# Performance work log

Measured on AMD Instinct MI355X. Metric: run time of the kernel, lower is better.

## Reference

```python
import jax, jax.numpy as jnp
import numpy as np

B, T, N, H = 32, 12, 1024, 64


def _norm_laplacian(A):
    # I - D^{-1/2} A D^{-1/2}
    d = A.sum(axis=1)
    d_is = jnp.where(d > 0, d ** -0.5, 0.0)
    return jnp.eye(A.shape[0], dtype=A.dtype) - d_is[:, None] * A * d_is[None, :]


def setup_inputs() -> dict:
    key = jax.random.key(0)
    ks = jax.random.split(key, 8)
    inputs = jax.random.normal(ks[0], (B, T, N), jnp.float32)
    states = jax.random.normal(ks[1], (T, B, N * H), jnp.float32) * 0.1
    dtw = jax.random.uniform(ks[2], (N, N), jnp.float32)
    adj = jax.random.uniform(ks[3], (N, N), jnp.float32)
    spectrum = jax.random.uniform(ks[4], (N, N), jnp.float32)
    time_delay = jax.random.normal(ks[5], (N, N), jnp.float32) * 10.0
    lim1 = (6.0 / (H + 1 + 2 * H)) ** 0.5  # xavier_uniform
    W1 = jax.random.uniform(ks[6], (H + 1, 2 * H), jnp.float32, -lim1, lim1)
    b1 = jnp.ones((2 * H,), jnp.float32)  # bias init 1.0 for conv1
    lim2 = (6.0 / (H + 1 + H)) ** 0.5
    W2 = jax.random.uniform(ks[7], (H + 1, H), jnp.float32, -lim2, lim2)
    b2 = jnp.zeros((H,), jnp.float32)
    return {"inputs": inputs, "states": states, "dtw": dtw, "adj": adj,
            "spectrum": spectrum, "time_delay": time_delay,
            "W1": W1, "b1": b1, "W2": W2, "b2": b2, "sample_rate": 5}


def reference(inputs, states, dtw, adj, spectrum, time_delay, W1, b1, W2, b2, sample_rate):
    Bs, Ts, Nn = inputs.shape
    Hh = W2.shape[1]
    I = jnp.eye(Nn, dtype=jnp.float32)
    L_adj = _norm_laplacian(adj)
    L_spec = _norm_laplacian(spectrum)
    # time_indicator = times - ceil(|td| / sample_rate)
    time_ind = jnp.float32(Ts) - jnp.ceil(jnp.abs(time_delay) / sample_rate)

    def gconv(A, x, h3, W, b):
        # x: [B,N], h3: [B,N,H'] -> [B, N*out]
        cat = jnp.concatenate([x[..., None], h3], axis=-1)          # [B,N,H'+1]
        a = jnp.einsum('mn,bnk->bmk', A, cat)                       # [B,N,H'+1]
        return (a @ W + b).reshape(Bs, -1)

    def step(carry, xs):
        gcn1, gcn2, _ = carry
        t, x, h = xs                                                # x:[B,N], h:[B,N*H]
        multi = t == Ts - 1
        dtwt = jnp.where((dtw != 0) & ((t + 1) > time_ind), dtw, 0.0)
        A = jnp.where(multi,
                      (dtwt + I + L_adj + L_spec) / 3.0,
                      (dtwt + L_spec + I) / 2.0)
        gcn1 = gcn1 + gconv(A, x, h.reshape(Bs, Nn, Hh), W1, b1)
        ru = jax.nn.sigmoid(gcn1)
        r, u = jnp.split(ru, 2, axis=1)
        gcn2 = gcn2 + gconv(A, x, (r * h).reshape(Bs, Nn, Hh), W2, b2)
        c = jnp.tanh(gcn2)
        h_new = u * h + (1.0 - u) * c
        return (gcn1, gcn2, h_new), None

    init = (jnp.zeros((Bs, Nn * 2 * Hh), jnp.float32),
            jnp.zeros((Bs, Nn * Hh), jnp.float32),
            jnp.zeros((Bs, Nn * Hh), jnp.float32))
    x_t = jnp.transpose(inputs, (1, 0, 2))                          # [T,B,N]
    (_, _, h_new), _ = jax.lax.scan(step, init, (jnp.arange(Ts), x_t, states))
    return (h_new, h_new)
```

## Files before the change

kernel.cpp:

```cpp
#include <hip/hip_runtime.h>
#include <math.h>

#define NN 1024
#define BB 32
#define TT 12
#define HH 64
#define K1 65
#define NCOLS (BB * K1)
#define BPAD 72
#define NC2 (BB * BPAD)
#define NH (NN * HH)
#define KX 1024
#define BM 128
#define BN 256
#define BKK 32
#define NBUF 3
#define PTS 264

typedef __attribute__((ext_vector_type(8))) _Float16 h8;
typedef __attribute__((ext_vector_type(4))) float f32x4;

__device__ __forceinline__ void gload16(const void* g, void* l) {
    __builtin_amdgcn_global_load_lds((__attribute__((address_space(1))) void*)g,
                                     (__attribute__((address_space(3))) void*)l,
                                     16, 0, 0);
}

__global__ void rowsum_rsqrt(const float* __restrict__ M, float* __restrict__ ds) {
    int row = blockIdx.x;
    const float* p = M + (size_t)row * NN;
    float s = 0.f;
    for (int i = threadIdx.x; i < NN; i += blockDim.x) s += p[i];
    __shared__ float red[256];
    red[threadIdx.x] = s;
    __syncthreads();
    for (int off = 128; off; off >>= 1) {
        if (threadIdx.x < off) red[threadIdx.x] += red[threadIdx.x + off];
        __syncthreads();
    }
    if (threadIdx.x == 0) {
        float d = red[0];
        ds[row] = d > 0.f ? 1.0f / sqrtf(d) : 0.f;
    }
}

__global__ void build_A2(const float* __restrict__ dtw, const float* __restrict__ adj,
                         const float* __restrict__ spec, const float* __restrict__ td,
                         const float* __restrict__ dsA, const float* __restrict__ dsS,
                         const int* __restrict__ sr_ptr, _Float16* __restrict__ A2) {
    int idx = blockIdx.x * blockDim.x + threadIdx.x;
    int m = idx >> 10, n = idx & 1023;
    float sr = (float)sr_ptr[0];
    float dtw_v = dtw[idx], adj_v = adj[idx], spec_v = spec[idx], td_v = td[idx];
    float I = (m == n) ? 1.f : 0.f;
    float Lspec = I - dsS[m] * spec_v * dsS[n];
    float Ladj  = I - dsA[m] * adj_v * dsA[n];
    float tind = (float)TT - ceilf(fabsf(td_v) / sr);
    float base2 = 0.5f * (Lspec + I);
    float base3 = (Lspec + Ladj + I) * (1.f / 3.f);
    bool nz = (dtw_v != 0.f);
#pragma unroll
    for (int t = 0; t < TT; ++t) {
        bool act = nz && ((float)(t + 1) > tind);
        float a = (t == TT - 1) ? base3 + (act ? dtw_v * (1.f / 3.f) : 0.f)
                                : base2 + (act ? dtw_v * 0.5f : 0.f);
        A2[((size_t)t * NN + m) * KX + n] = (_Float16)a;
    }
}

__global__ __launch_bounds__(256) void build_cat(
    const float* __restrict__ inputs, const float* __restrict__ states,
    const _Float16* __restrict__ rall, _Float16* __restrict__ cat,
    int tbase, int pass2) {
    __shared__ float hs[64][68];
    __shared__ float rs[64][68];
    const int z = blockIdx.z, t = tbase + z;
    const int b = blockIdx.y, nb = blockIdx.x;
    const int tid = threadIdx.x;
    const float* sb = states + ((size_t)t * BB + b) * NH + (size_t)nb * 4096;
    const float4* src = (const float4*)sb;
#pragma unroll
    for (int q = 0; q < 4; ++q) {
        float4 v = src[tid * 4 + q];
        int fi = tid * 16 + q * 4;
        *(float4*)&hs[fi >> 6][fi & 63] = v;
    }
    if (pass2) {
        const _Float16* rb = rall + ((size_t)t * BB + b) * NH + (size_t)nb * 4096;
#pragma unroll
        for (int i = 0; i < 16; ++i) {
            int fi = tid * 16 + i;
            rs[fi >> 6][fi & 63] = (float)rb[fi];
        }
    }
    __syncthreads();
    _Float16* catz = cat + (size_t)z * NC2 * KX;
    int jp = tid >> 2, ni = (tid & 3) << 4;
    int col = b * BPAD + 1 + jp;
    __attribute__((aligned(16))) _Float16 hib[16];
#pragma unroll
    for (int i = 0; i < 16; ++i) {
        float v = hs[ni + i][jp];
        if (pass2) v *= rs[ni + i][jp];
        hib[i] = (_Float16)v;
    }
    size_t dst = (size_t)col * KX + nb * 64 + ni;
    *(uint4*)(catz + dst)     = *(uint4*)&hib[0];
    *(uint4*)(catz + dst + 8) = *(uint4*)&hib[8];
    if (tid < 64) {
        float v = inputs[((size_t)b * TT + t) * NN + nb * 64 + tid];
        catz[(size_t)(b * BPAD) * KX + nb * 64 + tid] = (_Float16)v;
    }
}

__global__ __launch_bounds__(256) void scale_cat(
    const _Float16* __restrict__ rall, _Float16* __restrict__ cat, int tbase) {
    __shared__ float rs[64][68];
    const int z = blockIdx.z, t = tbase + z;
    const int b = blockIdx.y, nb = blockIdx.x;
    const int tid = threadIdx.x;
    const _Float16* rb = rall + ((size_t)t * BB + b) * NH + (size_t)nb * 4096;
    {
        h8 r0 = *(const h8*)(rb + tid * 16);
        h8 r1 = *(const h8*)(rb + tid * 16 + 8);
        int node = tid >> 2, c0 = (tid & 3) << 4;
#pragma unroll
        for (int i = 0; i < 8; ++i) {
            rs[node][c0 + i]     = (float)r0[i];
            rs[node][c0 + 8 + i] = (float)r1[i];
        }
    }
    __syncthreads();
    _Float16* catz = cat + (size_t)z * NC2 * KX;
    const int jp = tid >> 2, ni = (tid & 3) << 4;
    const int col = b * BPAD + 1 + jp;
    size_t dst = (size_t)col * KX + nb * 64 + ni;
    h8 v0 = *(const h8*)(catz + dst);
    h8 v1 = *(const h8*)(catz + dst + 8);
    h8 o0, o1;
#pragma unroll
    for (int i = 0; i < 8; ++i) {
        o0[i] = (_Float16)((float)v0[i] * rs[ni + i][jp]);
        o1[i] = (_Float16)((float)v1[i] * rs[ni + 8 + i][jp]);
    }
    *(h8*)(catz + dst)     = o0;
    *(h8*)(catz + dst + 8) = o1;
}

__global__ __launch_bounds__(256, 2) void gemm_f16(
    const _Float16* __restrict__ A2, const _Float16* __restrict__ cat,
    _Float16* __restrict__ P, int tbase) {
    __shared__ __align__(16) _Float16 smem[NBUF * (BM + BN) * BKK];
    _Float16* Asb = smem;
    _Float16* Xsb = smem + NBUF * BM * BKK;
    const int tid = threadIdx.x;
    const int lane = tid & 63;
    const int wid = tid >> 6;
    int bid = blockIdx.x;
    int l = (bid & 7) * ((int)gridDim.x >> 3) + (bid >> 3);
    int z = l / 72; int r = l - z * 72;
    int bx = r >> 3;
    int by = r & 7;
    const int m0 = by * BM;
    const int n0 = bx * BN;
    const _Float16* Ab = A2 + (size_t)(tbase + z) * NN * KX + (size_t)m0 * KX;
    const _Float16* Xb = cat + (size_t)z * NC2 * KX + (size_t)n0 * KX;

    f32x4 acc[8][4];
#pragma unroll
    for (int i = 0; i < 8; ++i)
#pragma unroll
        for (int j = 0; j < 4; ++j) acc[i][j] = {0.f, 0.f, 0.f, 0.f};

    const int wn = wid << 6;
    const int fl = lane & 15;
    const int fh = lane >> 4;

    auto stage = [&](int buf, int k0) {
#pragma unroll
        for (int c = 0; c < 2; ++c) {
            int p = c * 256 + tid;
            int row = p & 127;
            int kg  = p >> 7;
            gload16(Ab + (size_t)row * KX + k0 + kg * 8, &Asb[(size_t)(buf * BM * BKK + p * 8)]);
        }
#pragma unroll
        for (int c = 0; c < 4; ++c) {
            int p = c * 256 + tid;
            int row = p & 255;
            int kg  = p >> 8;
            gload16(Xb + (size_t)row * KX + k0 + kg * 8, &Xsb[(size_t)(buf * BN * BKK + p * 8)]);
        }
    };
    auto compute = [&](int buf) {
        h8 a[8], x[4];
#pragma unroll
        for (int i = 0; i < 8; ++i)
            a[i] = *(const h8*)&Asb[(size_t)(buf * BM * BKK + ((fh << 7) + (i << 4) + fl) * 8)];
#pragma unroll
        for (int j = 0; j < 4; ++j)
            x[j] = *(const h8*)&Xsb[(size_t)(buf * BN * BKK + ((fh << 8) + wn + (j << 4) + fl) * 8)];
#pragma unroll
        for (int i = 0; i < 8; ++i)
#pragma unroll
            for (int j = 0; j < 4; ++j)
                acc[i][j] = __builtin_amdgcn_mfma_f32_16x16x32_f16(a[i], x[j], acc[i][j], 0, 0, 0);
    };

    stage(0, 0);
    stage(1, BKK);
    const int nk = KX / BKK;
    for (int it = 0; it < nk; ++it) {
        const int cur = it % 3;
        if (it + 2 < nk) {
            stage((it + 2) % 3, (it + 2) * BKK);
            asm volatile("s_waitcnt vmcnt(12)" ::: "memory");
        } else if (it + 1 < nk) {
            asm volatile("s_waitcnt vmcnt(6)" ::: "memory");
        } else {
            asm volatile("s_waitcnt vmcnt(0)" ::: "memory");
        }
        __builtin_amdgcn_s_barrier();
        compute(cur);
        __builtin_amdgcn_s_barrier();
    }

    _Float16* Pt = smem;
#pragma unroll
    for (int i = 0; i < 8; ++i)
#pragma unroll
        for (int r4 = 0; r4 < 4; ++r4) {
            int row = (i << 4) + (fh << 2) + r4;
#pragma unroll
            for (int j = 0; j < 4; ++j)
                Pt[row * PTS + wn + (j << 4) + fl] = (_Float16)acc[i][j][r4];
        }
    __syncthreads();
    _Float16* Pz = P + (size_t)z * NN * NC2;
    const int rr = tid >> 5;
    const int cc = tid & 31;
#pragma unroll
    for (int c = 0; c < 16; ++c) {
        int row = rr + (c << 3);
        uint4 v = *(const uint4*)&Pt[row * PTS + cc * 8];
        *(uint4*)(Pz + (size_t)(m0 + row) * NC2 + n0 + cc * 8) = v;
    }
}

__global__ __launch_bounds__(256) void stage2m(const _Float16* __restrict__ P,
                                               const float* __restrict__ W,
                                               const float* __restrict__ bias,
                                               float* __restrict__ cum,
                                               _Float16* __restrict__ rall,
                                               int tbase, int zc) {
    __shared__ __align__(16) _Float16 Pl[TT * NC2];
    __shared__ _Float16 Wl[K1 * 128];
    const int m = blockIdx.x;
    const int tid = threadIdx.x;
    const int lane = tid & 63, wid = tid >> 6;
    const int fl = lane & 15, fh = lane >> 4;
    for (int i = tid; i < K1 * 128; i += 256) Wl[i] = (_Float16)W[i];
    const int chunks = zc * (NC2 / 8);
    for (int idx = tid; idx < chunks; idx += 256) {
        int z = idx / (NC2 / 8), off = idx - z * (NC2 / 8);
        gload16(P + ((size_t)z * NN + m) * NC2 + off * 8, (char*)Pl + (size_t)idx * 16);
    }
    __syncthreads();
    const int nt0 = wid * 2;
    h8 wf[2][2];
    float w64[2], bvv[2];
#pragma unroll
    for (int n2 = 0; n2 < 2; ++n2) {
        int k2 = (nt0 + n2) * 16 + fl;
        w64[n2] = (float)Wl[64 * 128 + k2];
        bvv[n2] = bias[k2];
#pragma unroll
        for (int ks = 0; ks < 2; ++ks) {
            h8 tmp;
#pragma unroll
            for (int j = 0; j < 8; ++j)
                tmp[j] = Wl[(ks * 32 + fh * 8 + j) * 128 + k2];
            wf[n2][ks] = tmp;
        }
    }
    f32x4 g[2][2];
    if (tbase > 0) {
#pragma unroll
        for (int mt = 0; mt < 2; ++mt)
#pragma unroll
            for (int n2 = 0; n2 < 2; ++n2)
#pragma unroll
                for (int r4 = 0; r4 < 4; ++r4) {
                    int b = mt * 16 + fh * 4 + r4;
                    int k2 = (nt0 + n2) * 16 + fl;
                    g[mt][n2][r4] = cum[(size_t)b * (2 * NH) + (size_t)m * 128 + k2];
                }
    } else {
#pragma unroll
        for (int mt = 0; mt < 2; ++mt)
#pragma unroll
            for (int n2 = 0; n2 < 2; ++n2)
                g[mt][n2] = {0.f, 0.f, 0.f, 0.f};
    }
#pragma unroll 1
    for (int z = 0; z < zc; ++z) {
        const _Float16* Pz = &Pl[z * NC2];
        h8 af[2][2];
#pragma unroll
        for (int mt = 0; mt < 2; ++mt)
#pragma unroll
            for (int ks = 0; ks < 2; ++ks)
                af[mt][ks] = *(const h8*)&Pz[(mt * 16 + fl) * BPAD + ks * 32 + fh * 8];
#pragma unroll
        for (int mt = 0; mt < 2; ++mt)
#pragma unroll
            for (int n2 = 0; n2 < 2; ++n2)
#pragma unroll
                for (int ks = 0; ks < 2; ++ks)
                    g[mt][n2] = __builtin_amdgcn_mfma_f32_16x16x32_f16(
                        af[mt][ks], wf[n2][ks], g[mt][n2], 0, 0, 0);
        float p64[2][4];
#pragma unroll
        for (int mt = 0; mt < 2; ++mt)
#pragma unroll
            for (int r4 = 0; r4 < 4; ++r4)
                p64[mt][r4] = (float)Pz[(mt * 16 + fh * 4 + r4) * BPAD + 64];
#pragma unroll
        for (int mt = 0; mt < 2; ++mt)
#pragma unroll
            for (int n2 = 0; n2 < 2; ++n2)
#pragma unroll
                for (int r4 = 0; r4 < 4; ++r4)
                    g[mt][n2][r4] += p64[mt][r4] * w64[n2] + bvv[n2];
        if (m < 512) {
            const int t = tbase + z;
#pragma unroll
            for (int mt = 0; mt < 2; ++mt)
#pragma unroll
                for (int n2 = 0; n2 < 2; ++n2)
#pragma unroll
                    for (int r4 = 0; r4 < 4; ++r4) {
                        int b = mt * 16 + fh * 4 + r4;
                        int k2 = (nt0 + n2) * 16 + fl;
                        float rv = 1.f / (1.f + expf(-g[mt][n2][r4]));
                        rall[((size_t)t * BB + b) * NH + (size_t)m * 128 + k2] = (_Float16)rv;
                    }
        }
    }
    if (m >= 512 || tbase + zc < TT) {
#pragma unroll
        for (int mt = 0; mt < 2; ++mt)
#pragma unroll
            for (int n2 = 0; n2 < 2; ++n2)
#pragma unroll
                for (int r4 = 0; r4 < 4; ++r4) {
                    int b = mt * 16 + fh * 4 + r4;
                    int k2 = (nt0 + n2) * 16 + fl;
                    cum[(size_t)b * (2 * NH) + (size_t)m * 128 + k2] = g[mt][n2][r4];
                }
    }
}

__global__ __launch_bounds__(128) void stage2p2f(const _Float16* __restrict__ P,
                                                 const float* __restrict__ W,
                                                 const float* __restrict__ bias,
                                                 const float* __restrict__ cum1,
                                                 const float* __restrict__ states,
                                                 float* __restrict__ out, int zc) {
    __shared__ float Pl[K1][37];
    __shared__ float Wl[K1 * 64];
    const int m = blockIdx.x;
    for (int i = threadIdx.x; i < K1 * 64; i += 128) Wl[i] = W[i];
    for (int i = threadIdx.x; i < NCOLS; i += 128) {
        int b = i / K1, k = i - b * K1;
        float s = 0.f;
        for (int z = 0; z < zc; ++z)
            s += (float)P[((size_t)z * NN + m) * NC2 + b * BPAD + k];
        Pl[k][b] = s;
    }
    __syncthreads();
    const int k2q = (threadIdx.x & 15) << 2;
    const int bq4 = (threadIdx.x >> 4) << 2;
    const float4 bv = *(const float4*)(bias + k2q);

    for (int bi = 0; bi < 4; ++bi) {
        const int b = bq4 + bi;
        float a0 = 0.f, a1 = 0.f, a2 = 0.f, a3 = 0.f;
#pragma unroll 4
        for (int k = 0; k < K1; ++k) {
            float p = Pl[k][b];
            float4 w4 = *(const float4*)&Wl[k * 64 + k2q];
            a0 += p * w4.x; a1 += p * w4.y; a2 += p * w4.z; a3 += p * w4.w;
        }
        const int f = m * HH + k2q;
        float g0 = a0 + zc * bv.x, g1 = a1 + zc * bv.y;
        float g2 = a2 + zc * bv.z, g3 = a3 + zc * bv.w;
        const float4 ul = *(const float4*)(cum1 + (size_t)b * 2 * NH + NH + f);
        const float4 hv = *(const float4*)(states + ((size_t)(TT - 1) * BB + b) * NH + f);
        float4 ov;
        {
            float u = 1.f / (1.f + expf(-ul.x)); ov.x = u * hv.x + (1.f - u) * tanhf(g0);
        }
        {
            float u = 1.f / (1.f + expf(-ul.y)); ov.y = u * hv.y + (1.f - u) * tanhf(g1);
        }
        {
            float u = 1.f / (1.f + expf(-ul.z)); ov.z = u * hv.z + (1.f - u) * tanhf(g2);
        }
        {
            float u = 1.f / (1.f + expf(-ul.w)); ov.w = u * hv.w + (1.f - u) * tanhf(g3);
        }
        *(float4*)(out + (size_t)b * NH + f) = ov;
        *(float4*)(out + (size_t)BB * NH + (size_t)b * NH + f) = ov;
    }
}

__global__ __launch_bounds__(128) void stage2p2(const _Float16* __restrict__ P,
                                                const float* __restrict__ W,
                                                const float* __restrict__ bias,
                                                float* __restrict__ cum, int zc) {
    __shared__ float Pl[K1][37];
    __shared__ float Wl[K1 * 64];
    const int m = blockIdx.x;
    for (int i = threadIdx.x; i < K1 * 64; i += 128) Wl[i] = W[i];
    for (int i = threadIdx.x; i < NCOLS; i += 128) {
        int b = i / K1, k = i - b * K1;
        float s = 0.f;
        for (int z = 0; z < zc; ++z)
            s += (float)P[((size_t)z * NN + m) * NC2 + b * BPAD + k];
        Pl[k][b] = s;
    }
    __syncthreads();
    const int k2q = (threadIdx.x & 15) << 2;
    const int bq4 = (threadIdx.x >> 4) << 2;
    const float4 bv = *(const float4*)(bias + k2q);

    for (int bi = 0; bi < 4; ++bi) {
        const int b = bq4 + bi;
        float a0 = 0.f, a1 = 0.f, a2 = 0.f, a3 = 0.f;
#pragma unroll 4
        for (int k = 0; k < K1; ++k) {
            float p = Pl[k][b];
            float4 w4 = *(const float4*)&Wl[k * 64 + k2q];
            a0 += p * w4.x; a1 += p * w4.y; a2 += p * w4.z; a3 += p * w4.w;
        }
        float* cp = cum + (size_t)b * NN * 64 + (size_t)m * 64 + k2q;
        float4 c4 = *(float4*)cp;
        c4.x += a0 + zc * bv.x; c4.y += a1 + zc * bv.y;
        c4.z += a2 + zc * bv.z; c4.w += a3 + zc * bv.w;
        *(float4*)cp = c4;
    }
}

__global__ void finalize(const float* __restrict__ cum1, const float* __restrict__ cum2,
                         const float* __restrict__ states, float* __restrict__ out) {
    int idx = blockIdx.x * blockDim.x + threadIdx.x;
    if (idx >= BB * NH) return;
    int b = idx >> 16;
    int f = idx & (NH - 1);
    float u = 1.f / (1.f + expf(-cum1[(size_t)b * 2 * NH + NH + f]));
    float h = states[((size_t)(TT - 1) * BB + b) * NH + f];
    float c = tanhf(cum2[idx]);
    float o = u * h + (1.f - u) * c;
    out[idx] = o;
    out[(size_t)BB * NH + idx] = o;
}

extern "C" void kernel_launch(void* const* d_in, const int* in_sizes, int n_in,
                              void* d_out, int out_size, void* d_ws, size_t ws_size,
                              hipStream_t stream) {
    const float* inputs = (const float*)d_in[0];
    const float* states = (const float*)d_in[1];
    const float* dtw    = (const float*)d_in[2];
    const float* adj    = (const float*)d_in[3];
    const float* spec   = (const float*)d_in[4];
    const float* td     = (const float*)d_in[5];
    const float* W1     = (const float*)d_in[6];
    const float* b1     = (const float*)d_in[7];
    const float* W2     = (const float*)d_in[8];
    const float* b2     = (const float*)d_in[9];
    const int*   sr     = (const int*)d_in[10];
    float* out = (float*)d_out;

    char* ws = (char*)d_ws;
    const size_t szA2   = (size_t)TT * NN * KX * 2;
    const size_t szCum1 = (size_t)BB * 2 * NH * 4;
    const size_t szCum2 = (size_t)BB * NH * 4;
    const size_t szRall = (size_t)TT * BB * NH * 2;

    _Float16* A2  = (_Float16*)ws;
    float* cum1 = (float*)(ws + szA2);
    float* cum2 = (float*)(ws + szA2 + szCum1);
    float* dsA  = (float*)(ws + szA2 + szCum1 + szCum2);
    float* dsS  = (float*)(ws + szA2 + szCum1 + szCum2 + 4096);
    _Float16* rall = (_Float16*)(ws + szA2 + szCum1 + szCum2 + 8192);
    size_t offRest = szA2 + szCum1 + szCum2 + 8192 + szRall;

    rowsum_rsqrt<<<NN, 256, 0, stream>>>(adj, dsA);
    rowsum_rsqrt<<<NN, 256, 0, stream>>>(spec, dsS);
    build_A2<<<(NN * NN) / 256, 256, 0, stream>>>(dtw, adj, spec, td, dsA, dsS, sr, A2);

    const size_t szCatZ = (size_t)NC2 * KX * 2;
    const size_t szPZ   = (size_t)NN * NC2 * 2;
    int C;
    if      (ws_size >= offRest + 12 * (szCatZ + szPZ)) C = 12;
    else if (ws_size >= offRest + 4 * (szCatZ + szPZ))  C = 4;
    else                                                C = 1;
    _Float16* cat = (_Float16*)(ws + offRest);
    _Float16* P16 = (_Float16*)(ws + offRest + (size_t)C * szCatZ);

    if (C == 12) {
        build_cat<<<dim3(16, 32, 12), 256, 0, stream>>>(inputs, states, nullptr, cat, 0, 0);
        gemm_f16<<<dim3(72 * 12), 256, 0, stream>>>(A2, cat, P16, 0);
        stage2m<<<NN, 256, 0, stream>>>(P16, W1, b1, cum1, rall, 0, 12);
        scale_cat<<<dim3(16, 32, 12), 256, 0, stream>>>(rall, cat, 0);
        gemm_f16<<<dim3(72 * 12), 256, 0, stream>>>(A2, cat, P16, 0);
        stage2p2f<<<NN, 128, 0, stream>>>(P16, W2, b2, cum1, states, out, 12);
    } else {
        hipMemsetAsync(cum2, 0, szCum2, stream);
        for (int tb = 0; tb < TT; tb += C) {
            build_cat<<<dim3(16, 32, C), 256, 0, stream>>>(inputs, states, nullptr, cat, tb, 0);
            gemm_f16<<<dim3(72 * C), 256, 0, stream>>>(A2, cat, P16, tb);
            stage2m<<<NN, 256, 0, stream>>>(P16, W1, b1, cum1, rall, tb, C);
        }
        for (int tb = 0; tb < TT; tb += C) {
            build_cat<<<dim3(16, 32, C), 256, 0, stream>>>(inputs, states, rall, cat, tb, 1);
            gemm_f16<<<dim3(72 * C), 256, 0, stream>>>(A2, cat, P16, tb);
            stage2p2<<<NN, 128, 0, stream>>>(P16, W2, b2, cum2, C);
        }
        finalize<<<(BB * NH + 255) / 256, 256, 0, stream>>>(cum1, cum2, states, out);
    }
}
```

Measured before the change: 400.2 us.

## Replace GEMM with 256x256-tile 8-wave kernel using 4-slot prefetch pipeline

Replaces the 128x256-tile, 4-wave GEMM with a 256x256-tile, 512-thread kernel. It uses a 4-slot LDS ring buffer with a three-stage prefetch, split-phase MFMA issue with s_setprio, and an epilogue that writes the output in two halves. The larger tile raises arithmetic intensity per block and halves the block count. In exchange, occupancy drops to one block per CU and the 432-block grid leaves a partial last wave on the CUs. A cosmetic reformat of stage2p2f is also included.

```diff
diff --git a/kernel.cpp b/kernel.cpp
--- a/kernel.cpp
+++ b/kernel.cpp
@@ -11,11 +11,8 @@
 #define NC2 (BB * BPAD)
 #define NH (NN * HH)
 #define KX 1024
-#define BM 128
-#define BN 256
-#define BKK 32
-#define NBUF 3
 #define PTS 264
+#define SLOT 16384
 
 typedef __attribute__((ext_vector_type(8))) _Float16 h8;
 typedef __attribute__((ext_vector_type(4))) float f32x4;
@@ -147,22 +144,27 @@
     *(h8*)(catz + dst + 8) = o1;
 }
 
-__global__ __launch_bounds__(256, 2) void gemm_f16(
+__global__ __launch_bounds__(512, 1) void gemm8p(
     const _Float16* __restrict__ A2, const _Float16* __restrict__ cat,
     _Float16* __restrict__ P, int tbase) {
-    __shared__ __align__(16) _Float16 smem[NBUF * (BM + BN) * BKK];
-    _Float16* Asb = smem;
-    _Float16* Xsb = smem + NBUF * BM * BKK;
+    __shared__ __align__(16) _Float16 smem[4 * SLOT];
     const int tid = threadIdx.x;
     const int lane = tid & 63;
     const int wid = tid >> 6;
+    const int wr = wid >> 2;
+    const int wc = wid & 3;
+    const int fl = lane & 15, fh = lane >> 4;
+
     int bid = blockIdx.x;
-    int l = (bid & 7) * ((int)gridDim.x >> 3) + (bid >> 3);
-    int z = l / 72; int r = l - z * 72;
-    int bx = r >> 3;
-    int by = r & 7;
-    const int m0 = by * BM;
-    const int n0 = bx * BN;
+    int l;
+    if (((int)gridDim.x & 7) == 0)
+        l = (bid & 7) * ((int)gridDim.x >> 3) + (bid >> 3);
+    else
+        l = bid;
+    int z = l / 36; int r = l - z * 36;
+    int by = r & 3;
+    int bx = r >> 2;
+    const int m0 = by * 256, n0 = bx * 256;
     const _Float16* Ab = A2 + (size_t)(tbase + z) * NN * KX + (size_t)m0 * KX;
     const _Float16* Xb = cat + (size_t)z * NC2 * KX + (size_t)n0 * KX;
 
@@ -172,78 +174,89 @@
 #pragma unroll
         for (int j = 0; j < 4; ++j) acc[i][j] = {0.f, 0.f, 0.f, 0.f};
 
-    const int wn = wid << 6;
-    const int fl = lane & 15;
-    const int fh = lane >> 4;
-
-    auto stage = [&](int buf, int k0) {
+    auto stage = [&](int s) {
+        const int slot = s & 3;
+        const int k0 = s * 32;
 #pragma unroll
         for (int c = 0; c < 2; ++c) {
-            int p = c * 256 + tid;
-            int row = p & 127;
-            int kg  = p >> 7;
-            gload16(Ab + (size_t)row * KX + k0 + kg * 8, &Asb[(size_t)(buf * BM * BKK + p * 8)]);
-        }
-#pragma unroll
-        for (int c = 0; c < 4; ++c) {
-            int p = c * 256 + tid;
-            int row = p & 255;
-            int kg  = p >> 8;
-            gload16(Xb + (size_t)row * KX + k0 + kg * 8, &Xsb[(size_t)(buf * BN * BKK + p * 8)]);
+            int u = c * 512 + tid;
+            int kg = u >> 8;
+            int row = u & 255;
+            gload16(Ab + (size_t)row * KX + k0 + kg * 8, &smem[(size_t)(slot * SLOT + u * 8)]);
+            gload16(Xb + (size_t)row * KX + k0 + kg * 8, &smem[(size_t)(slot * SLOT + 8192 + u * 8)]);
         }
     };
-    auto compute = [&](int buf) {
-        h8 a[8], x[4];
-#pragma unroll
-        for (int i = 0; i < 8; ++i)
-            a[i] = *(const h8*)&Asb[(size_t)(buf * BM * BKK + ((fh << 7) + (i << 4) + fl) * 8)];
-#pragma unroll
-        for (int j = 0; j < 4; ++j)
-            x[j] = *(const h8*)&Xsb[(size_t)(buf * BN * BKK + ((fh << 8) + wn + (j << 4) + fl) * 8)];
-#pragma unroll
-        for (int i = 0; i < 8; ++i)
+
+    h8 xf[4];
+    auto phase = [&](int slot, int half, bool withX) {
+        h8 a[4];
+        const int abase = slot * SLOT + (fh * 256 + wr * 128 + half * 64 + fl) * 8;
+#pragma unroll
+        for (int ii = 0; ii < 4; ++ii)
+            a[ii] = *(const h8*)&smem[abase + ii * 128];
+        if (withX) {
+            const int xbase = slot * SLOT + 8192 + (fh * 256 + wc * 64 + fl) * 8;
 #pragma unroll
             for (int j = 0; j < 4; ++j)
-                acc[i][j] = __builtin_amdgcn_mfma_f32_16x16x32_f16(a[i], x[j], acc[i][j], 0, 0, 0);
+                xf[j] = *(const h8*)&smem[xbase + j * 128];
+        }
+        __builtin_amdgcn_s_setprio(1);
+#pragma unroll
+        for (int ii = 0; ii < 4; ++ii)
+#pragma unroll
+            for (int j = 0; j < 4; ++j)
+                acc[half * 4 + ii][j] =
+                    __builtin_amdgcn_mfma_f32_16x16x32_f16(a[ii], xf[j], acc[half * 4 + ii][j], 0, 0, 0);
+        __builtin_amdgcn_s_setprio(0);
     };
 
-    stage(0, 0);
-    stage(1, BKK);
-    const int nk = KX / BKK;
-    for (int it = 0; it < nk; ++it) {
-        const int cur = it % 3;
-        if (it + 2 < nk) {
-            stage((it + 2) % 3, (it + 2) * BKK);
-            asm volatile("s_waitcnt vmcnt(12)" ::: "memory");
-        } else if (it + 1 < nk) {
-            asm volatile("s_waitcnt vmcnt(6)" ::: "memory");
-        } else {
-            asm volatile("s_waitcnt vmcnt(0)" ::: "memory");
-        }
+    stage(0); stage(1); stage(2);
+    for (int t = 0; t < 15; ++t) {
+        const int s0 = 2 * t;
+        asm volatile("s_waitcnt vmcnt(8)" ::: "memory");
         __builtin_amdgcn_s_barrier();
-        compute(cur);
+        stage(s0 + 3);
+        phase(s0 & 3, 0, true);
+        phase(s0 & 3, 1, false);
+        asm volatile("s_waitcnt vmcnt(8)" ::: "memory");
         __builtin_amdgcn_s_barrier();
-    }
-
-    _Float16* Pt = smem;
-#pragma unroll
-    for (int i = 0; i < 8; ++i)
-#pragma unroll
-        for (int r4 = 0; r4 < 4; ++r4) {
-            int row = (i << 4) + (fh << 2) + r4;
-#pragma unroll
-            for (int j = 0; j < 4; ++j)
-                Pt[row * PTS + wn + (j << 4) + fl] = (_Float16)acc[i][j][r4];
-        }
-    __syncthreads();
+        if (t < 14) stage(s0 + 4);
+        phase((s0 + 1) & 3, 0, true);
+        phase((s0 + 1) & 3, 1, false);
+    }
+    asm volatile("s_waitcnt vmcnt(4)" ::: "memory");
+    __builtin_amdgcn_s_barrier();
+    phase(30 & 3, 0, true);
+    phase(30 & 3, 1, false);
+    asm volatile("s_waitcnt vmcnt(0)" ::: "memory");
+    __builtin_amdgcn_s_barrier();
+    phase(31 & 3, 0, true);
+    phase(31 & 3, 1, false);
+
     _Float16* Pz = P + (size_t)z * NN * NC2;
-    const int rr = tid >> 5;
-    const int cc = tid & 31;
-#pragma unroll
-    for (int c = 0; c < 16; ++c) {
-        int row = rr + (c << 3);
-        uint4 v = *(const uint4*)&Pt[row * PTS + cc * 8];
-        *(uint4*)(Pz + (size_t)(m0 + row) * NC2 + n0 + cc * 8) = v;
+#pragma unroll
+    for (int h = 0; h < 2; ++h) {
+        __syncthreads();
+        if (wr == h) {
+#pragma unroll
+            for (int i = 0; i < 8; ++i)
+#pragma unroll
+                for (int r4 = 0; r4 < 4; ++r4) {
+                    int rl = (i << 4) + (fh << 2) + r4;
+#pragma unroll
+                    for (int j = 0; j < 4; ++j)
+                        smem[rl * PTS + (wc << 6) + (j << 4) + fl] = (_Float16)acc[i][j][r4];
+                }
+        }
+        __syncthreads();
+#pragma unroll
+        for (int c = 0; c < 8; ++c) {
+            int u = c * 512 + tid;
+            int rl = u >> 5;
+            int cc = u & 31;
+            uint4 v = *(const uint4*)&smem[rl * PTS + cc * 8];
+            *(uint4*)(Pz + (size_t)(m0 + h * 128 + rl) * NC2 + n0 + cc * 8) = v;
+        }
     }
 }
 
@@ -398,18 +411,10 @@
         const float4 ul = *(const float4*)(cum1 + (size_t)b * 2 * NH + NH + f);
         const float4 hv = *(const float4*)(states + ((size_t)(TT - 1) * BB + b) * NH + f);
         float4 ov;
-        {
-            float u = 1.f / (1.f + expf(-ul.x)); ov.x = u * hv.x + (1.f - u) * tanhf(g0);
-        }
-        {
-            float u = 1.f / (1.f + expf(-ul.y)); ov.y = u * hv.y + (1.f - u) * tanhf(g1);
-        }
-        {
-            float u = 1.f / (1.f + expf(-ul.z)); ov.z = u * hv.z + (1.f - u) * tanhf(g2);
-        }
-        {
-            float u = 1.f / (1.f + expf(-ul.w)); ov.w = u * hv.w + (1.f - u) * tanhf(g3);
-        }
+        { float u = 1.f / (1.f + expf(-ul.x)); ov.x = u * hv.x + (1.f - u) * tanhf(g0); }
+        { float u = 1.f / (1.f + expf(-ul.y)); ov.y = u * hv.y + (1.f - u) * tanhf(g1); }
+        { float u = 1.f / (1.f + expf(-ul.z)); ov.z = u * hv.z + (1.f - u) * tanhf(g2); }
+        { float u = 1.f / (1.f + expf(-ul.w)); ov.w = u * hv.w + (1.f - u) * tanhf(g3); }
         *(float4*)(out + (size_t)b * NH + f) = ov;
         *(float4*)(out + (size_t)BB * NH + (size_t)b * NH + f) = ov;
     }
@@ -511,21 +516,21 @@
 
     if (C == 12) {
         build_cat<<<dim3(16, 32, 12), 256, 0, stream>>>(inputs, states, nullptr, cat, 0, 0);
-        gemm_f16<<<dim3(72 * 12), 256, 0, stream>>>(A2, cat, P16, 0);
+        gemm8p<<<dim3(36 * 12), 512, 0, stream>>>(A2, cat, P16, 0);
         stage2m<<<NN, 256, 0, stream>>>(P16, W1, b1, cum1, rall, 0, 12);
         scale_cat<<<dim3(16, 32, 12), 256, 0, stream>>>(rall, cat, 0);
-        gemm_f16<<<dim3(72 * 12), 256, 0, stream>>>(A2, cat, P16, 0);
+        gemm8p<<<dim3(36 * 12), 512, 0, stream>>>(A2, cat, P16, 0);
         stage2p2f<<<NN, 128, 0, stream>>>(P16, W2, b2, cum1, states, out, 12);
     } else {
         hipMemsetAsync(cum2, 0, szCum2, stream);
         for (int tb = 0; tb < TT; tb += C) {
             build_cat<<<dim3(16, 32, C), 256, 0, stream>>>(inputs, states, nullptr, cat, tb, 0);
-            gemm_f16<<<dim3(72 * C), 256, 0, stream>>>(A2, cat, P16, tb);
+            gemm8p<<<dim3(36 * C), 512, 0, stream>>>(A2, cat, P16, tb);
             stage2m<<<NN, 256, 0, stream>>>(P16, W1, b1, cum1, rall, tb, C);
         }
         for (int tb = 0; tb < TT; tb += C) {
             build_cat<<<dim3(16, 32, C), 256, 0, stream>>>(inputs, states, rall, cat, tb, 1);
-            gemm_f16<<<dim3(72 * C), 256, 0, stream>>>(A2, cat, P16, tb);
+            gemm8p<<<dim3(36 * C), 512, 0, stream>>>(A2, cat, P16, tb);
             stage2p2<<<NN, 128, 0, stream>>>(P16, W2, b2, cum2, C);
         }
         finalize<<<(BB * NH + 255) / 256, 256, 0, stream>>>(cum1, cum2, states, out);
```

Measured after the change: 442.0 us. 10.4% more time.
